# Kernel optimization log

Measured on AMD Instinct MI355X. Metric: run time of the kernel, lower is better.

## Reference

```python
import jax, jax.numpy as jnp
import numpy as np


def setup_inputs() -> dict:
    key = jax.random.key(0)
    ks = jax.random.split(key, 8)
    B, dz, K, N, dx, T = 64, 16, 16, 1024, 128, 500
    # initial latent state [n_trials, dz, k_particles]
    z0 = jax.random.normal(ks[0], (B, dz, K), jnp.float32)
    # per-latent leak/time-constant A = (1 - dt/tau), kept in (0.8, 0.99) for stability
    A = jax.random.uniform(ks[1], (dz,), jnp.float32, minval=0.8, maxval=0.99)
    # low-rank recurrent factors: n [dz, N] (right), m [N, dz] (left)
    n = jax.random.normal(ks[2], (dz, N), jnp.float32) * (1.0 / N)
    m = jax.random.normal(ks[3], (N, dz), jnp.float32) * (1.0 / np.sqrt(dz))
    # neuron bias h [N], latent bias hz [dz]
    h = jax.random.normal(ks[4], (N,), jnp.float32) * 0.1
    hz = jax.random.normal(ks[5], (dz,), jnp.float32) * 0.01
    # readout B [dz, dx] ~ sqrt(2/dy) randn, bias initialised to zero (as in Observation)
    Bobs = jax.random.normal(ks[6], (dz, dx), jnp.float32) * np.sqrt(2.0 / dz)
    Bias = jnp.zeros((dx,), jnp.float32)
    return {"z0": z0, "A": A, "n": n, "m": m, "h": h, "hz": hz,
            "Bobs": Bobs, "Bias": Bias, "T": T}


def reference(z0, A, n, m, h, hz, Bobs, Bias, T):
    """Low-rank RNN rolled out for T steps + linear (identity-nonlin) readout.

    Per step (Transition.forward with relu nonlinearity, weight_scaler=1, du=0):
        R   = relu(m @ z - h)                       # rates, [B, N, K]
        z'  = A * z + n @ R + hz                    # [B, dz, K]
    Readout (Observation.forward, identity nonlinearity):
        X = einsum('zx,bzTK->bxTK', Bobs, zs) + Bias
    """
    Ab = A[None, :, None]      # [1, dz, 1]
    hb = h[None, :, None]      # [1, N, 1]
    hzb = hz[None, :, None]    # [1, dz, 1]

    def step(z, _):
        X = jnp.einsum('Nz,bzk->bNk', m, z)           # project to neurons
        R = jax.nn.relu(X - hb)                       # rates
        z_new = Ab * z + jnp.einsum('zN,bNk->bzk', n, R) + hzb
        return z_new, z_new

    _, zs = jax.lax.scan(step, z0, None, length=T)    # [T, B, dz, K]
    zs = jnp.transpose(zs, (1, 2, 0, 3))              # [B, dz, T, K]
    # Observation readout
    X = jnp.einsum('zx,bzTK->bxTK', Bobs, zs) + Bias[None, :, None, None]
    return X
```

## Files before the change

### kernel.cpp

```cpp
#include <hip/hip_runtime.h>
#include <hip/hip_bf16.h>


typedef __attribute__((ext_vector_type(4))) short short4v;
typedef __attribute__((ext_vector_type(8))) short short8v;
typedef __attribute__((ext_vector_type(4))) float float4v;

#define BB 64
#define DZ 16
#define KC 16
#define NN 1024
#define DX 128
#define NW 8
#define ITER (NN / (16 * NW))
#define NH (ITER / 2)

#define BARRIER_LGKM() asm volatile("s_waitcnt lgkmcnt(0)\n\ts_barrier" ::: "memory")

union FragAB {
  short4v s;
  __hip_bfloat162 h2[2];
};
union Frag8 {
  short8v s8;
  short4v s4[2];
};

__device__ inline short4v pack_bf16x4(float a, float b, float c, float d) {
  FragAB u;
  u.h2[0] = __float22bfloat162_rn(make_float2(a, b));
  u.h2[1] = __float22bfloat162_rn(make_float2(c, d));
  return u.s;
}

__device__ inline float4v mfma_bf16(short4v a, short4v b, float4v c) {
#if __has_builtin(__builtin_amdgcn_mfma_f32_16x16x16bf16_1k)
  return __builtin_amdgcn_mfma_f32_16x16x16bf16_1k(a, b, c, 0, 0, 0);
#else
  float4v d;
  asm("v_mfma_f32_16x16x16_bf16 %0, %1, %2, %3"
      : "=v"(d) : "v"(a), "v"(b), "v"(c));
  return d;
#endif
}

__device__ inline float4v mfma_bf16_x32(short8v a, short8v b, float4v c) {
#if __has_builtin(__builtin_amdgcn_mfma_f32_16x16x32_bf16)
  return __builtin_amdgcn_mfma_f32_16x16x32_bf16(a, b, c, 0, 0, 0);
#else
  float4v d;
  asm("v_mfma_f32_16x16x32_bf16 %0, %1, %2, %3"
      : "=v"(d) : "v"(a), "v"(b), "v"(c));
  return d;
#endif
}

__global__ __launch_bounds__(64 * NW, 2)
void lrrnn_fused(const float* __restrict__ z0, const float* __restrict__ Adec,
                 const float* __restrict__ nmat, const float* __restrict__ mmat,
                 const float* __restrict__ hvec, const float* __restrict__ hzvec,
                 const float* __restrict__ Bobs, const float* __restrict__ Bias,
                 const int* __restrict__ Tptr, float* __restrict__ out)
{
  const int T    = Tptr[0];
  const int b    = blockIdx.x;
  const int tid  = threadIdx.x;
  const int wave = tid >> 6;
  const int lane = tid & 63;
  const int g    = lane >> 4;
  const int c    = lane & 15;

  __shared__ float4v part[NW][64];
  __shared__ short4v zbuf[64];

  FragAB mf[ITER];
  Frag8  nf8[NH];
  float4v negH[ITER];
#pragma unroll
  for (int i = 0; i < ITER; ++i) {
    const int rowbase = wave * (16 * ITER) + i * 16;
    float4v mv = *(const float4v*)(mmat + (rowbase + c) * DZ + g * 4);
    mf[i].s = pack_bf16x4(mv[0], mv[1], mv[2], mv[3]);
    float4v hv = *(const float4v*)(hvec + rowbase + g * 4);
    negH[i][0] = -hv[0]; negH[i][1] = -hv[1];
    negH[i][2] = -hv[2]; negH[i][3] = -hv[3];
  }
#pragma unroll
  for (int i = 0; i < NH; ++i) {
    const int rb0 = wave * (16 * ITER) + (2 * i) * 16;
    float4v nv0 = *(const float4v*)(nmat + c * NN + rb0 + g * 4);
    float4v nv1 = *(const float4v*)(nmat + c * NN + rb0 + 16 + g * 4);
    nf8[i].s4[0] = pack_bf16x4(nv0[0], nv0[1], nv0[2], nv0[3]);
    nf8[i].s4[1] = pack_bf16x4(nv1[0], nv1[1], nv1[2], nv1[3]);
  }

  const float4v Af  = *(const float4v*)(Adec + g * 4);
  const float4v hzf = *(const float4v*)(hzvec + g * 4);
  const float4v zerov = {0.f, 0.f, 0.f, 0.f};

  const int t0 = (wave >= 1) ? (wave - 1) : 0;
  const int nt = (wave == 1) ? 2 : ((wave == 0) ? 0 : 1);
  int tiles[2] = {t0, 7};
  FragAB bobsF[2];
  float4v biasF[2];
  unsigned oof[2];
#pragma unroll
  for (int s = 0; s < 2; ++s) {
    const int xb = tiles[s] * 16;
    bobsF[s].s = pack_bf16x4(Bobs[(4 * g + 0) * DX + xb + c],
                             Bobs[(4 * g + 1) * DX + xb + c],
                             Bobs[(4 * g + 2) * DX + xb + c],
                             Bobs[(4 * g + 3) * DX + xb + c]);
    const float bx = Bias[xb + c];
    biasF[s][0] = bx; biasF[s][1] = bx; biasF[s][2] = bx; biasF[s][3] = bx;
    oof[s] = (unsigned)(b * DX + xb + c) * (unsigned)T * KC + (unsigned)(g * 4);
  }

  float4v zf;
#pragma unroll
  for (int j = 0; j < 4; ++j)
    zf[j] = z0[b * DZ * KC + (g * 4 + j) * KC + c];
  FragAB zb;
  zb.s = pack_bf16x4(zf[0], zf[1], zf[2], zf[3]);

  for (int t = 0; t < T; ++t) {
    float4v xv[ITER];
#pragma unroll
    for (int i = 0; i < ITER; ++i)
      xv[i] = mfma_bf16(mf[i].s, zb.s, negH[i]);

    Frag8 R8[NH];
#pragma unroll
    for (int i = 0; i < NH; ++i) {
      const float4v x0 = xv[2 * i], x1 = xv[2 * i + 1];
      R8[i].s4[0] = pack_bf16x4(fmaxf(x0[0], 0.f), fmaxf(x0[1], 0.f),
                                fmaxf(x0[2], 0.f), fmaxf(x0[3], 0.f));
      R8[i].s4[1] = pack_bf16x4(fmaxf(x1[0], 0.f), fmaxf(x1[1], 0.f),
                                fmaxf(x1[2], 0.f), fmaxf(x1[3], 0.f));
    }

    float4v a0 = mfma_bf16_x32(nf8[0].s8, R8[0].s8, (wave == 0) ? hzf : zerov);
    float4v a1 = mfma_bf16_x32(nf8[1].s8, R8[1].s8, zerov);
    a0 = mfma_bf16_x32(nf8[2].s8, R8[2].s8, a0);
    a1 = mfma_bf16_x32(nf8[3].s8, R8[3].s8, a1);
    const float4v zp = a0 + a1;

    if (wave != 0) part[wave][lane] = zp;
    BARRIER_LGKM();

    if (wave == 0) {
      const float4v p1 = part[1][lane];
      const float4v p2 = part[2][lane];
      const float4v p3 = part[3][lane];
      const float4v p4 = part[4][lane];
      const float4v p5 = part[5][lane];
      const float4v p6 = part[6][lane];
      const float4v p7 = part[7][lane];
      const float4v tot = ((zp + p1) + (p2 + p3)) + ((p4 + p5) + (p6 + p7));
#pragma unroll
      for (int j = 0; j < 4; ++j)
        zf[j] = fmaf(Af[j], zf[j], tot[j]);
      zb.s = pack_bf16x4(zf[0], zf[1], zf[2], zf[3]);
      zbuf[lane] = zb.s;
    } else if (t > 0) {
      const unsigned tk = (unsigned)(t - 1) * KC;
#pragma unroll
      for (int s = 0; s < 2; ++s) {
        if (s < nt) {
          float4v o = mfma_bf16(zb.s, bobsF[s].s, biasF[s]);
          *(float4v*)(out + oof[s] + tk) = o;
        }
      }
    }
    BARRIER_LGKM();

    if (wave != 0) zb.s = zbuf[lane];
  }

  if (wave != 0) {
    const unsigned tk = (unsigned)(T - 1) * KC;
#pragma unroll
    for (int s = 0; s < 2; ++s) {
      if (s < nt) {
        float4v o = mfma_bf16(zb.s, bobsF[s].s, biasF[s]);
        *(float4v*)(out + oof[s] + tk) = o;
      }
    }
  }
}

extern "C" void kernel_launch(void* const* d_in, const int* in_sizes, int n_in,
                              void* d_out, int out_size, void* d_ws, size_t ws_size,
                              hipStream_t stream) {
  const float* z0   = (const float*)d_in[0];
  const float* A    = (const float*)d_in[1];
  const float* nmat = (const float*)d_in[2];
  const float* mmat = (const float*)d_in[3];
  const float* h    = (const float*)d_in[4];
  const float* hz   = (const float*)d_in[5];
  const float* Bobs = (const float*)d_in[6];
  const float* Bias = (const float*)d_in[7];
  const int*   T    = (const int*)d_in[8];
  (void)in_sizes; (void)n_in; (void)out_size; (void)d_ws; (void)ws_size;
  lrrnn_fused<<<dim3(BB), dim3(64 * NW), 0, stream>>>(
      z0, A, nmat, mmat, h, hz, Bobs, Bias, T, (float*)d_out);
}
```

Before: 323.3 us.

## Split recurrence and readout into separate kernels via workspace z history

The fused kernel is split in two. One kernel runs the recurrence and writes the bf16 z state for every step to workspace. A second, highly parallel kernel then computes the Bobs readout and output stores over time chunks. This takes the 32 MB of output stores off the serial recurrence critical path, at the cost of an extra kernel launch and a round trip of the z history through memory. T is now derived from out_size on the host instead of being read on the device, and the old fused kernel is kept as a fallback when workspace is too small.

```diff
diff --git a/kernel.cpp b/kernel.cpp
--- a/kernel.cpp
+++ b/kernel.cpp
@@ -14,6 +14,7 @@
 #define NW 8
 #define ITER (NN / (16 * NW))
 #define NH (ITER / 2)
+#define CS 50
 
 #define BARRIER_LGKM() asm volatile("s_waitcnt lgkmcnt(0)\n\ts_barrier" ::: "memory")
 
@@ -56,13 +57,11 @@
 }
 
 __global__ __launch_bounds__(64 * NW, 2)
-void lrrnn_fused(const float* __restrict__ z0, const float* __restrict__ Adec,
+void lrrnn_recur(const float* __restrict__ z0, const float* __restrict__ Adec,
                  const float* __restrict__ nmat, const float* __restrict__ mmat,
                  const float* __restrict__ hvec, const float* __restrict__ hzvec,
-                 const float* __restrict__ Bobs, const float* __restrict__ Bias,
-                 const int* __restrict__ Tptr, float* __restrict__ out)
+                 int T, short4v* __restrict__ zhist)
 {
-  const int T    = Tptr[0];
   const int b    = blockIdx.x;
   const int tid  = threadIdx.x;
   const int wave = tid >> 6;
@@ -98,9 +97,151 @@
   const float4v hzf = *(const float4v*)(hzvec + g * 4);
   const float4v zerov = {0.f, 0.f, 0.f, 0.f};
 
-  const int t0 = (wave >= 1) ? (wave - 1) : 0;
+  float4v zf;
+#pragma unroll
+  for (int j = 0; j < 4; ++j)
+    zf[j] = z0[b * DZ * KC + (g * 4 + j) * KC + c];
+  FragAB zb;
+  zb.s = pack_bf16x4(zf[0], zf[1], zf[2], zf[3]);
+
+  short4v* zh = zhist + (size_t)b * T * 64 + lane;
+
+  for (int t = 0; t < T; ++t) {
+    float4v xv[ITER];
+#pragma unroll
+    for (int i = 0; i < ITER; ++i)
+      xv[i] = mfma_bf16(mf[i].s, zb.s, negH[i]);
+
+    Frag8 R8[NH];
+#pragma unroll
+    for (int i = 0; i < NH; ++i) {
+      const float4v x0 = xv[2 * i], x1 = xv[2 * i + 1];
+      R8[i].s4[0] = pack_bf16x4(fmaxf(x0[0], 0.f), fmaxf(x0[1], 0.f),
+                                fmaxf(x0[2], 0.f), fmaxf(x0[3], 0.f));
+      R8[i].s4[1] = pack_bf16x4(fmaxf(x1[0], 0.f), fmaxf(x1[1], 0.f),
+                                fmaxf(x1[2], 0.f), fmaxf(x1[3], 0.f));
+    }
+
+    float4v a0 = mfma_bf16_x32(nf8[0].s8, R8[0].s8, (wave == 0) ? hzf : zerov);
+    float4v a1 = mfma_bf16_x32(nf8[1].s8, R8[1].s8, zerov);
+    a0 = mfma_bf16_x32(nf8[2].s8, R8[2].s8, a0);
+    a1 = mfma_bf16_x32(nf8[3].s8, R8[3].s8, a1);
+    const float4v zp = a0 + a1;
+
+    if (wave != 0) part[wave][lane] = zp;
+    BARRIER_LGKM();
+
+    if (wave == 0) {
+      const float4v p1 = part[1][lane];
+      const float4v p2 = part[2][lane];
+      const float4v p3 = part[3][lane];
+      const float4v p4 = part[4][lane];
+      const float4v p5 = part[5][lane];
+      const float4v p6 = part[6][lane];
+      const float4v p7 = part[7][lane];
+      const float4v tot = ((zp + p1) + (p2 + p3)) + ((p4 + p5) + (p6 + p7));
+#pragma unroll
+      for (int j = 0; j < 4; ++j)
+        zf[j] = fmaf(Af[j], zf[j], tot[j]);
+      zb.s = pack_bf16x4(zf[0], zf[1], zf[2], zf[3]);
+      zbuf[lane] = zb.s;
+    }
+    BARRIER_LGKM();
+
+    if (wave != 0) zb.s = zbuf[lane];
+    if (wave == 1) zh[t * 64] = zb.s;
+  }
+}
+
+__global__ __launch_bounds__(256, 4)
+void lrrnn_readout(const short4v* __restrict__ zhist,
+                   const float* __restrict__ Bobs, const float* __restrict__ Bias,
+                   int T, int tch, float* __restrict__ out)
+{
+  const int bx   = blockIdx.x;
+  const int b    = bx / tch;
+  const int ch   = bx - b * tch;
+  const int tid  = threadIdx.x;
+  const int wave = tid >> 6;
+  const int lane = tid & 63;
+  const int g    = lane >> 4;
+  const int c    = lane & 15;
+
+  FragAB bobsF[2];
+  float4v biasF[2];
+  unsigned oof[2];
+#pragma unroll
+  for (int s = 0; s < 2; ++s) {
+    const int xb = (wave * 2 + s) * 16;
+    bobsF[s].s = pack_bf16x4(Bobs[(4 * g + 0) * DX + xb + c],
+                             Bobs[(4 * g + 1) * DX + xb + c],
+                             Bobs[(4 * g + 2) * DX + xb + c],
+                             Bobs[(4 * g + 3) * DX + xb + c]);
+    const float bxv = Bias[xb + c];
+    biasF[s][0] = bxv; biasF[s][1] = bxv; biasF[s][2] = bxv; biasF[s][3] = bxv;
+    oof[s] = (unsigned)(b * DX + xb + c) * (unsigned)T * KC + (unsigned)(g * 4);
+  }
+
+  const short4v* zh = zhist + (size_t)b * T * 64 + lane;
+  const int t0 = ch * CS;
+  const int t1 = (t0 + CS < T) ? (t0 + CS) : T;
+
+  for (int t = t0; t < t1; ++t) {
+    const short4v za = zh[t * 64];
+    const unsigned tk = (unsigned)t * KC;
+#pragma unroll
+    for (int s = 0; s < 2; ++s) {
+      float4v o = mfma_bf16(za, bobsF[s].s, biasF[s]);
+      *(float4v*)(out + oof[s] + tk) = o;
+    }
+  }
+}
+
+__global__ __launch_bounds__(64 * NW, 2)
+void lrrnn_mono(const float* __restrict__ z0, const float* __restrict__ Adec,
+                const float* __restrict__ nmat, const float* __restrict__ mmat,
+                const float* __restrict__ hvec, const float* __restrict__ hzvec,
+                const float* __restrict__ Bobs, const float* __restrict__ Bias,
+                int T, float* __restrict__ out)
+{
+  const int b    = blockIdx.x;
+  const int tid  = threadIdx.x;
+  const int wave = tid >> 6;
+  const int lane = tid & 63;
+  const int g    = lane >> 4;
+  const int c    = lane & 15;
+
+  __shared__ float4v part[NW][64];
+  __shared__ short4v zbuf[64];
+
+  FragAB mf[ITER];
+  Frag8  nf8[NH];
+  float4v negH[ITER];
+#pragma unroll
+  for (int i = 0; i < ITER; ++i) {
+    const int rowbase = wave * (16 * ITER) + i * 16;
+    float4v mv = *(const float4v*)(mmat + (rowbase + c) * DZ + g * 4);
+    mf[i].s = pack_bf16x4(mv[0], mv[1], mv[2], mv[3]);
+    float4v hv = *(const float4v*)(hvec + rowbase + g * 4);
+    negH[i][0] = -hv[0]; negH[i][1] = -hv[1];
+    negH[i][2] = -hv[2]; negH[i][3] = -hv[3];
+  }
+#pragma unroll
+  for (int i = 0; i < NH; ++i) {
+    const int rb0 = wave * (16 * ITER) + (2 * i) * 16;
+    float4v nv0 = *(const float4v*)(nmat + c * NN + rb0 + g * 4);
+    float4v nv1 = *(const float4v*)(nmat + c * NN + rb0 + 16 + g * 4);
+    nf8[i].s4[0] = pack_bf16x4(nv0[0], nv0[1], nv0[2], nv0[3]);
+    nf8[i].s4[1] = pack_bf16x4(nv1[0], nv1[1], nv1[2], nv1[3]);
+  }
+
+  const float4v Af  = *(const float4v*)(Adec + g * 4);
+  const float4v hzf = *(const float4v*)(hzvec + g * 4);
+  const float4v zerov = {0.f, 0.f, 0.f, 0.f};
+
+  const int t0i = (wave >= 1) ? (wave - 1) : 0;
   const int nt = (wave == 1) ? 2 : ((wave == 0) ? 0 : 1);
-  int tiles[2] = {t0, 7};
+  int tiles[2] = {t0i, 7};
   FragAB bobsF[2];
   float4v biasF[2];
   unsigned oof[2];
@@ -111,8 +252,8 @@
                              Bobs[(4 * g + 1) * DX + xb + c],
                              Bobs[(4 * g + 2) * DX + xb + c],
                              Bobs[(4 * g + 3) * DX + xb + c]);
-    const float bx = Bias[xb + c];
-    biasF[s][0] = bx; biasF[s][1] = bx; biasF[s][2] = bx; biasF[s][3] = bx;
+    const float bxv = Bias[xb + c];
+    biasF[s][0] = bxv; biasF[s][1] = bxv; biasF[s][2] = bxv; biasF[s][3] = bxv;
     oof[s] = (unsigned)(b * DX + xb + c) * (unsigned)T * KC + (unsigned)(g * 4);
   }
 
@@ -200,8 +341,20 @@
   const float* hz   = (const float*)d_in[5];
   const float* Bobs = (const float*)d_in[6];
   const float* Bias = (const float*)d_in[7];
-  const int*   T    = (const int*)d_in[8];
-  (void)in_sizes; (void)n_in; (void)out_size; (void)d_ws; (void)ws_size;
-  lrrnn_fused<<<dim3(BB), dim3(64 * NW), 0, stream>>>(
-      z0, A, nmat, mmat, h, hz, Bobs, Bias, T, (float*)d_out);
-}
+  (void)in_sizes; (void)n_in;
+
+  const int T = out_size / (BB * DX * KC);
+  const size_t need = (size_t)BB * T * 64 * sizeof(short4v);
+
+  if (ws_size >= need) {
+    short4v* zhist = (short4v*)d_ws;
+    lrrnn_recur<<<dim3(BB), dim3(64 * NW), 0, stream>>>(
+        z0, A, nmat, mmat, h, hz, T, zhist);
+    const int tch = (T + CS - 1) / CS;
+    lrrnn_readout<<<dim3(BB * tch), dim3(256), 0, stream>>>(
+        zhist, Bobs, Bias, T, tch, (float*)d_out);
+  } else {
+    lrrnn_mono<<<dim3(BB), dim3(64 * NW), 0, stream>>>(
+        z0, A, nmat, mmat, h, hz, Bobs, Bias, T, (float*)d_out);
+  }
+}
```

Result: slower. 398.5 us (+23.2%).

## Split neuron dimension across 16 waves per block instead of 8

Applied to the files above, without the earlier changes.

Doubles the waves per block from 8 to 16, so each wave handles half as many neurons per step: four rank-16 MFMAs and two K=32 MFMAs instead of eight and four. This shortens the per-step serial MFMA chain on the critical path of the recurrence. The cost is a wider cross-wave reduction in shared memory, where wave 0 now sums 15 partials, and more barrier participants. The readout tiles are spread one per wave over waves 1-8, replacing the uneven two-tile assignment.

```diff
diff --git a/kernel.cpp b/kernel.cpp
--- a/kernel.cpp
+++ b/kernel.cpp
@@ -11,7 +11,7 @@
 #define KC 16
 #define NN 1024
 #define DX 128
-#define NW 8
+#define NW 16
 #define ITER (NN / (16 * NW))
 #define NH (ITER / 2)
 
@@ -55,7 +55,7 @@
 #endif
 }
 
-__global__ __launch_bounds__(64 * NW, 2)
+__global__ __launch_bounds__(64 * NW, 1)
 void lrrnn_fused(const float* __restrict__ z0, const float* __restrict__ Adec,
                  const float* __restrict__ nmat, const float* __restrict__ mmat,
                  const float* __restrict__ hvec, const float* __restrict__ hzvec,
@@ -98,22 +98,22 @@
   const float4v hzf = *(const float4v*)(hzvec + g * 4);
   const float4v zerov = {0.f, 0.f, 0.f, 0.f};
 
-  const int t0 = (wave >= 1) ? (wave - 1) : 0;
-  const int nt = (wave == 1) ? 2 : ((wave == 0) ? 0 : 1);
-  int tiles[2] = {t0, 7};
-  FragAB bobsF[2];
-  float4v biasF[2];
-  unsigned oof[2];
-#pragma unroll
-  for (int s = 0; s < 2; ++s) {
-    const int xb = tiles[s] * 16;
-    bobsF[s].s = pack_bf16x4(Bobs[(4 * g + 0) * DX + xb + c],
-                             Bobs[(4 * g + 1) * DX + xb + c],
-                             Bobs[(4 * g + 2) * DX + xb + c],
-                             Bobs[(4 * g + 3) * DX + xb + c]);
-    const float bx = Bias[xb + c];
-    biasF[s][0] = bx; biasF[s][1] = bx; biasF[s][2] = bx; biasF[s][3] = bx;
-    oof[s] = (unsigned)(b * DX + xb + c) * (unsigned)T * KC + (unsigned)(g * 4);
+  const int nt = (wave >= 1 && wave <= 8) ? 1 : 0;
+  FragAB bobsF;
+  float4v biasF;
+  unsigned oof = 0;
+  if (nt) {
+    const int xb = (wave - 1) * 16;
+    bobsF.s = pack_bf16x4(Bobs[(4 * g + 0) * DX + xb + c],
+                          Bobs[(4 * g + 1) * DX + xb + c],
+                          Bobs[(4 * g + 2) * DX + xb + c],
+                          Bobs[(4 * g + 3) * DX + xb + c]);
+    const float bxv = Bias[xb + c];
+    biasF[0] = bxv; biasF[1] = bxv; biasF[2] = bxv; biasF[3] = bxv;
+    oof = (unsigned)(b * DX + xb + c) * (unsigned)T * KC + (unsigned)(g * 4);
+  } else {
+    bobsF.s = (short4v){0, 0, 0, 0};
+    biasF = zerov;
   }
 
   float4v zf;
@@ -141,51 +141,40 @@
 
     float4v a0 = mfma_bf16_x32(nf8[0].s8, R8[0].s8, (wave == 0) ? hzf : zerov);
     float4v a1 = mfma_bf16_x32(nf8[1].s8, R8[1].s8, zerov);
-    a0 = mfma_bf16_x32(nf8[2].s8, R8[2].s8, a0);
-    a1 = mfma_bf16_x32(nf8[3].s8, R8[3].s8, a1);
     const float4v zp = a0 + a1;
 
     if (wave != 0) part[wave][lane] = zp;
     BARRIER_LGKM();
 
     if (wave == 0) {
-      const float4v p1 = part[1][lane];
-      const float4v p2 = part[2][lane];
-      const float4v p3 = part[3][lane];
-      const float4v p4 = part[4][lane];
-      const float4v p5 = part[5][lane];
-      const float4v p6 = part[6][lane];
-      const float4v p7 = part[7][lane];
-      const float4v tot = ((zp + p1) + (p2 + p3)) + ((p4 + p5) + (p6 + p7));
+      const float4v p1  = part[1][lane],  p2  = part[2][lane];
+      const float4v p3  = part[3][lane],  p4  = part[4][lane];
+      const float4v p5  = part[5][lane],  p6  = part[6][lane];
+      const float4v p7  = part[7][lane],  p8  = part[8][lane];
+      const float4v p9  = part[9][lane],  p10 = part[10][lane];
+      const float4v p11 = part[11][lane], p12 = part[12][lane];
+      const float4v p13 = part[13][lane], p14 = part[14][lane];
+      const float4v p15 = part[15][lane];
+      const float4v s0 = ((zp + p1) + (p2 + p3)) + ((p4 + p5) + (p6 + p7));
+      const float4v s1 = ((p8 + p9) + (p10 + p11)) + ((p12 + p13) + (p14 + p15));
+      const float4v tot = s0 + s1;
 #pragma unroll
       for (int j = 0; j < 4; ++j)
         zf[j] = fmaf(Af[j], zf[j], tot[j]);
       zb.s = pack_bf16x4(zf[0], zf[1], zf[2], zf[3]);
       zbuf[lane] = zb.s;
-    } else if (t > 0) {
-      const unsigned tk = (unsigned)(t - 1) * KC;
-#pragma unroll
-      for (int s = 0; s < 2; ++s) {
-        if (s < nt) {
-          float4v o = mfma_bf16(zb.s, bobsF[s].s, biasF[s]);
-          *(float4v*)(out + oof[s] + tk) = o;
-        }
-      }
+    } else if (nt && t > 0) {
+      float4v o = mfma_bf16(zb.s, bobsF.s, biasF);
+      *(float4v*)(out + oof + (unsigned)(t - 1) * KC) = o;
     }
     BARRIER_LGKM();
 
     if (wave != 0) zb.s = zbuf[lane];
   }
 
-  if (wave != 0) {
-    const unsigned tk = (unsigned)(T - 1) * KC;
-#pragma unroll
-    for (int s = 0; s < 2; ++s) {
-      if (s < nt) {
-        float4v o = mfma_bf16(zb.s, bobsF[s].s, biasF[s]);
-        *(float4v*)(out + oof[s] + tk) = o;
-      }
-    }
+  if (nt) {
+    float4v o = mfma_bf16(zb.s, bobsF.s, biasF);
+    *(float4v*)(out + oof + (unsigned)(T - 1) * KC) = o;
   }
 }
 
```

Measured after the change: 356.6 us. 1.1x slower.
